# Optimization experiments

Hardware: AMD Instinct MI355X
Metric: run time of the kernel (lower is better)

## Reference

```python
import jax, jax.numpy as jnp
from jax import lax
import numpy as np

# ---- hyperparams (match init_kwargs) ----
NUM_HASHES = 8
BITS = 5
TABLE_SIZE = 64
M = 27            # ALSH augmentation length; M % (KH*KW) == 0
U = 0.83
KH = KW = 3
STRIDE = 1
PAD = 1
OUT_CHANNELS = 256
IN_CHANNELS = 64


def setup_inputs() -> dict:
    key = jax.random.key(0)
    k1, k2, k3 = jax.random.split(key, 3)
    x = jax.random.normal(k1, (32, IN_CHANNELS, 56, 56), jnp.float32)
    kernels = jax.random.normal(k2, (OUT_CHANNELS, IN_CHANNELS, KH, KW), jnp.float32) * 0.05
    a = jax.random.normal(k3, (NUM_HASHES * BITS, IN_CHANNELS * KH * KW + M), jnp.float32)
    return {"x": x, "kernels": kernels, "a": a}


def _scale_under_U(kv):
    # ScaleUnder_U: rescale all kernel vectors so max L2 norm == U
    norms = jnp.sqrt(jnp.sum(kv * kv, axis=1))
    return kv * (U / jnp.max(norms))


def _P(kv):
    # ALSH preprocessing: append ||x||^2, ||x||^4, ..., ||x||^(2^M)
    p = jnp.sum(kv * kv, axis=1, keepdims=True)  # ||x||^2
    cols = []
    for _ in range(M):
        cols.append(p)
        p = p * p
    return jnp.concatenate([kv] + cols, axis=1)  # [K, D+M]


_BIT_W = (2 ** jnp.arange(BITS)).astype(jnp.int32)


def _hash_vectors(a, v):
    # v: [K, D+M] -> bucket indices [NUM_HASHES, K]
    proj = v @ a.T                                   # [K, NUM_HASHES*BITS]
    bits = (proj > 0).astype(jnp.int32).reshape(-1, NUM_HASHES, BITS)
    idx = jnp.einsum('khb,b->hk', bits, _BIT_W)      # multi-bit SRP index
    return idx % TABLE_SIZE


def _build_table(bucket):
    # vectorized equivalent of the nested scalar-scatter loops in init_table:
    # append kernel id i to table[bucket[h, i]] in (h-major, i-minor) order.
    H, K = bucket.shape
    flat = bucket.reshape(-1)                        # [H*K]
    vals = (jnp.arange(H * K) % K).astype(jnp.int32) # stored value = kernel index i
    order = jnp.argsort(flat)                        # stable in jax
    sb, sv = flat[order], vals[order]
    pos = jnp.arange(H * K) - jnp.searchsorted(sb, sb, side='left')  # slot within bucket
    row_len = H * K
    table = jnp.zeros((TABLE_SIZE, row_len), jnp.int32).at[sb, pos].set(sv)
    lengths = jnp.zeros((TABLE_SIZE,), jnp.int32).at[flat].add(1)
    return table, lengths


def _vote_buckets(x, a):
    # Q: append M/(KH*KW) constant 1/2 planes; hash via convolution with a reshaped
    N, C, H, W = x.shape
    m_planes = M // (KH * KW)
    xq = jnp.concatenate([x, jnp.full((N, m_planes, H, W), 0.5, x.dtype)], axis=1)
    hk = a.reshape(NUM_HASHES * BITS, C + m_planes, KH, KW)  # a_to_kernel
    d = lax.conv_general_dilated(xq, hk, (STRIDE, STRIDE), [(PAD, PAD), (PAD, PAD)],
                                 dimension_numbers=('NCHW', 'OIHW', 'NCHW'))
    # [N, NUM_HASHES*BITS, H', W'] -> bucket per (hash fn, location)
    Np, _, Hp, Wp = d.shape
    bits = (d > 0).astype(jnp.int32).reshape(Np, NUM_HASHES, BITS, Hp * Wp)
    buckets = jnp.einsum('nhbs,b->hns', bits, _BIT_W) % TABLE_SIZE  # [H, N, S]
    return buckets.reshape(NUM_HASHES, -1)


def _active_mask(x, kernels, a):
    K = kernels.shape[0]
    kv = kernels.reshape(K, -1)
    buckets_k = _hash_vectors(a, _P(_scale_under_U(kv)))   # [H, K]
    table, lengths = _build_table(buckets_k)
    votes = _vote_buckets(x, a)                            # [H, N*S]
    tallied = jnp.zeros((NUM_HASHES, TABLE_SIZE), jnp.int32).at[
        jnp.arange(NUM_HASHES)[:, None], votes].add(1)     # count_votes
    indices = jnp.argmax(tallied, axis=1)                  # best bucket per hash fn
    entries = table[indices]                               # [H, row_len]
    valid = jnp.arange(table.shape[1])[None, :] < lengths[indices][:, None]
    # union of kernel ids across selected buckets (== sort+unique gather)
    mask = jnp.zeros((K,), jnp.float32).at[entries.reshape(-1)].max(
        valid.reshape(-1).astype(jnp.float32))
    return mask, tallied, indices


def reference(x, kernels, a):
    mask, tallied, indices = _active_mask(x, kernels, a)
    out = lax.conv_general_dilated(x, kernels, (STRIDE, STRIDE), [(PAD, PAD), (PAD, PAD)],
                                   dimension_numbers=('NCHW', 'OIHW', 'NCHW'))
    out = out * mask[None, :, None, None]  # conv restricted to the active kernel set
    return out, tallied, indices, mask
```

## Files before the change

### kernel.cpp

```cpp
#include <hip/hip_runtime.h>
#include <math.h>

#define NH 8
#define BITS_ 5
#define NB 40
#define TS 64
#define MAUG 27
#define CIN 64
#define HH 56
#define WW 56
#define NN 32
#define OCH 256
#define DK 576
#define DPM 603
#define HW (HH*WW)

#define CP 20
#define TILE 5440

typedef __attribute__((ext_vector_type(4))) float f32x4;
typedef __attribute__((ext_vector_type(8))) _Float16 f16x8;
typedef union { uint4 u; f16x8 h; } fragh_u;

__device__ __forceinline__ unsigned int f16b(float v) {
    union { _Float16 h; unsigned short u; } cv;
    cv.h = (_Float16)v;
    return (unsigned int)cv.u;
}
__device__ __forceinline__ float f16tof(unsigned int b) {
    union { _Float16 h; unsigned short u; } cv;
    cv.u = (unsigned short)b;
    return (float)cv.h;
}

__global__ void kP(const float* __restrict__ kern, const float* __restrict__ a,
                   float* __restrict__ aT, float* __restrict__ ctab,
                   int* __restrict__ tallied, float* __restrict__ normP,
                   unsigned short* __restrict__ whA,
                   unsigned short* __restrict__ vaH, unsigned short* __restrict__ vaL)
{
    const int bid = blockIdx.x;
    const int t = threadIdx.x;
    if (bid < 32) {
        for (int idx = bid * 256 + t; idx < DPM * NB; idx += 32 * 256) {
            int d = idx / NB, j = idx - d * NB;
            aT[idx] = a[j * DPM + d];
        }
    } else if (bid == 32) {
        for (int g = t; g < 9 * NB; g += 256) {
            int pat = g / NB, j = g - pat * NB;
            int ry = pat / 3, rx = pat % 3;
            float s = 0.f;
            for (int ky = 0; ky < 3; ++ky) {
                if (ry == 0 && ky == 0) continue;
                if (ry == 2 && ky == 2) continue;
                for (int kx = 0; kx < 3; ++kx) {
                    if (rx == 0 && kx == 0) continue;
                    if (rx == 2 && kx == 2) continue;
                    for (int mc = 0; mc < 3; ++mc)
                        s += a[j * DPM + DK + mc * 9 + ky * 3 + kx];
                }
            }
            ctab[g] = 0.5f * s;
        }
        for (int g = t; g < NH * TS; g += 256) tallied[g] = 0;
    } else if (bid < 37) {
        int g = (bid - 33) * 256 + t;
        int oc = g >> 2, part = g & 3;
        const float4* p = (const float4*)(kern + oc * DK + part * 144);
        float sq = 0.f;
        #pragma unroll 4
        for (int i = 0; i < 36; ++i) {
            float4 v = p[i];
            sq += v.x * v.x + v.y * v.y + v.z * v.z + v.w * v.w;
        }
        normP[g] = sq;
    } else {
        int idx = (bid - 37) * 256 + t;
        int f = idx >> 6, lane = idx & 63;
        if (f < 288) {
            const int kidxG = f >> 4, mf = f & 15;
            const int tap = kidxG % 9, cc = kidxG / 9;
            const int oc = mf * 16 + (lane & 15);
            const int cbase = cc * 32 + (lane >> 4) * 8;
            unsigned int hs[8];
            #pragma unroll
            for (int j = 0; j < 8; ++j)
                hs[j] = f16b(kern[oc * DK + (cbase + j) * 9 + tap]);
            unsigned int* p = (unsigned int*)(whA + ((size_t)f * 64 + lane) * 8);
            #pragma unroll
            for (int w2 = 0; w2 < 4; ++w2)
                p[w2] = hs[2 * w2] | (hs[2 * w2 + 1] << 16);
        } else if (f < 342) {
            const int fv = f - 288;
            const int kidxG = fv / 3, mfv = fv % 3;
            const int tap = kidxG % 9, cc = kidxG / 9;
            const int j = mfv * 16 + (lane & 15);
            const int cbase = cc * 32 + (lane >> 4) * 8;
            unsigned int hs[8], ls[8];
            #pragma unroll
            for (int jj = 0; jj < 8; ++jj) {
                float w = (j < NB) ? a[j * DPM + (cbase + jj) * 9 + tap] : 0.f;
                unsigned int h = f16b(w);
                unsigned int l = f16b(w - f16tof(h));
                hs[jj] = h; ls[jj] = l;
            }
            unsigned int* ph = (unsigned int*)(vaH + ((size_t)fv * 64 + lane) * 8);
            unsigned int* pl = (unsigned int*)(vaL + ((size_t)fv * 64 + lane) * 8);
            #pragma unroll
            for (int w2 = 0; w2 < 4; ++w2) {
                ph[w2] = hs[2 * w2] | (hs[2 * w2 + 1] << 16);
                pl[w2] = ls[2 * w2] | (ls[2 * w2 + 1] << 16);
            }
        }
    }
}

__global__ void __launch_bounds__(256) kH(const float* __restrict__ kern,
        const float* __restrict__ aT, const float* __restrict__ normP,
        int* __restrict__ bucket_k)
{
    __shared__ float xs[DK];
    __shared__ float red[256];
    __shared__ float accR[3 * 41];
    __shared__ float proj[NB];
    const int t = threadIdx.x;
    const int lane = t & 63, ty = t >> 6;
    const int oc = blockIdx.x;

    red[t] = fmaxf(fmaxf(normP[t], normP[t + 256]), fmaxf(normP[t + 512], normP[t + 768]));
    __syncthreads();
    for (int s = 128; s > 0; s >>= 1) {
        if (t < s) red[t] = fmaxf(red[t], red[t + s]);
        __syncthreads();
    }
    const float scale = 0.83f / sqrtf(red[0]);
    for (int i = t; i < DK; i += 256) xs[i] = scale * kern[(size_t)oc * DK + i];
    __syncthreads();

    const int j = (lane < NB) ? lane : (NB - 1);
    float acc = 0.f, sq = 0.f;
    const int d0 = ty * 144;
    for (int d = d0; d < d0 + 144; ++d) {
        float xv = xs[d];
        sq += xv * xv;
        acc += xv * aT[d * NB + j];
    }
    if (ty > 0) {
        if (lane < NB) accR[(ty - 1) * 41 + lane] = acc;
        if (lane == NB) accR[(ty - 1) * 41 + 40] = sq;
    }
    __syncthreads();
    if (ty == 0 && lane < NB) {
        acc += (accR[lane] + accR[41 + lane]) + accR[82 + lane];
        sq += (accR[40] + accR[81]) + accR[122];
        float pv = sq;
        for (int m = 0; m < MAUG; ++m) {
            acc += pv * aT[(DK + m) * NB + lane];
            pv = pv * pv;
        }
        proj[lane] = acc;
    }
    __syncthreads();
    if (t < NH) {
        int b = 0;
        #pragma unroll
        for (int bb = 0; bb < BITS_; ++bb)
            if (proj[t * BITS_ + bb] > 0.f) b |= (1 << bb);
        bucket_k[t * OCH + oc] = b & (TS - 1);
    }
}

template<int VOTE>
__global__ void __launch_bounds__(512) kM(const float* __restrict__ x,
        const unsigned short* __restrict__ whA,
        const unsigned short* __restrict__ vaH, const unsigned short* __restrict__ vaL,
        const float* __restrict__ ctab, int* __restrict__ tallied,
        const float* __restrict__ maskF, float* __restrict__ out)
{
    __shared__ unsigned int smem[2 * TILE];
    const int lane = threadIdx.x, wid = threadIdx.y;
    const int y0 = blockIdx.x * 2, n = blockIdx.y;
    const int mg = wid & 3, ng = wid >> 2;
    const int lcol = lane & 15, hi4 = lane >> 4;
    const int t = wid * 64 + lane;
    const int mfbase = VOTE ? 0 : 8;

    f32x4 acc[2][4];
    #pragma unroll
    for (int mfl = 0; mfl < 2; ++mfl)
        #pragma unroll
        for (int nf = 0; nf < 4; ++nf)
            acc[mfl][nf] = (f32x4){0.f, 0.f, 0.f, 0.f};
    f32x4 vacc[3];
    if (VOTE) {
        vacc[0] = (f32x4){0.f, 0.f, 0.f, 0.f};
        vacc[1] = (f32x4){0.f, 0.f, 0.f, 0.f};
        vacc[2] = (f32x4){0.f, 0.f, 0.f, 0.f};
    }

    if (t < 128) {
        int b = t & 3, tile = (t >> 2) & 1, li = (t >> 3) & 3, r = (t >> 5) & 3;
        int L = (li == 0) ? 0 : 64 + li;
        *(uint4*)&smem[tile * TILE + (r * 68 + L) * CP + b * 4] = make_uint4(0u, 0u, 0u, 0u);
    }

    const int q = lane;
    const int r = wid >> 1, half = wid & 1;
    const int y = y0 - 1 + r;
    const bool valid = (q < WW) && (y >= 0) && (y < HH);
    const int sbase = (r * 68 + q + 1) * CP + half * 8;

    for (int cc = 0; cc < 2; ++cc) {
        __syncthreads();
        {
            const float* xb = x + (((size_t)n * CIN + cc * 32 + half * 16) * HH +
                                   (valid ? y : 0)) * WW + q;
            #pragma unroll
            for (int u = 0; u < 2; ++u) {
                unsigned int dh[4], dl[4];
                #pragma unroll
                for (int dd = 0; dd < 4; ++dd) {
                    float v0 = valid ? xb[(size_t)(u * 8 + dd * 2) * HW] : 0.f;
                    float v1 = valid ? xb[(size_t)(u * 8 + dd * 2 + 1) * HW] : 0.f;
                    unsigned int h0 = f16b(v0), h1 = f16b(v1);
                    dh[dd] = h0 | (h1 << 16);
                    if (VOTE) {
                        unsigned int l0 = f16b(v0 - f16tof(h0));
                        unsigned int l1 = f16b(v1 - f16tof(h1));
                        dl[dd] = l0 | (l1 << 16);
                    }
                }
                *(uint4*)&smem[sbase + u * 4] = make_uint4(dh[0], dh[1], dh[2], dh[3]);
                if (VOTE)
                    *(uint4*)&smem[TILE + sbase + u * 4] = make_uint4(dl[0], dl[1], dl[2], dl[3]);
            }
        }
        __syncthreads();

        #pragma unroll
        for (int tap = 0; tap < 9; ++tap) {
            const int ky = tap / 3, kx = tap - ky * 3;
            const int kidx = cc * 9 + tap;
            fragh_u ah0, ah1;
            ah0.u = *(const uint4*)(whA + (((size_t)kidx * 16 + mfbase + mg * 2) * 64 + lane) * 8);
            ah1.u = *(const uint4*)(whA + (((size_t)kidx * 16 + mfbase + mg * 2 + 1) * 64 + lane) * 8);
            #pragma unroll
            for (int nf = 0; nf < 4; ++nf) {
                const int R = (ng + ky) * 68 + nf * 16 + lcol + kx;
                const int ad = R * CP + hi4 * 4;
                fragh_u bh;
                bh.u = *(const uint4*)&smem[ad];
                acc[0][nf] = __builtin_amdgcn_mfma_f32_16x16x32_f16(ah0.h, bh.h, acc[0][nf], 0, 0, 0);
                acc[1][nf] = __builtin_amdgcn_mfma_f32_16x16x32_f16(ah1.h, bh.h, acc[1][nf], 0, 0, 0);
                if (VOTE && nf == mg) {
                    fragh_u bl;
                    bl.u = *(const uint4*)&smem[TILE + ad];
                    #pragma unroll
                    for (int mfv = 0; mfv < 3; ++mfv) {
                        fragh_u vh, vl;
                        size_t fi = ((size_t)(kidx * 3 + mfv) * 64 + lane) * 8;
                        vh.u = *(const uint4*)(vaH + fi);
                        vl.u = *(const uint4*)(vaL + fi);
                        vacc[mfv] = __builtin_amdgcn_mfma_f32_16x16x32_f16(vh.h, bh.h, vacc[mfv], 0, 0, 0);
                        vacc[mfv] = __builtin_amdgcn_mfma_f32_16x16x32_f16(vh.h, bl.h, vacc[mfv], 0, 0, 0);
                        vacc[mfv] = __builtin_amdgcn_mfma_f32_16x16x32_f16(vl.h, bh.h, vacc[mfv], 0, 0, 0);
                    }
                }
            }
        }
    }

    const int yrow = y0 + ng;
    #pragma unroll
    for (int mfl = 0; mfl < 2; ++mfl) {
        #pragma unroll
        for (int reg = 0; reg < 4; ++reg) {
            const int oc = (mfbase + mg * 2 + mfl) * 16 + hi4 * 4 + reg;
            const float mv = VOTE ? 1.0f : maskF[oc];
            float* ob = out + (((size_t)n * OCH + oc) * HH + yrow) * WW;
            #pragma unroll
            for (int nf = 0; nf < 4; ++nf) {
                int col = nf * 16 + lcol;
                if (col < WW) ob[col] = acc[mfl][nf][reg] * mv;
            }
        }
    }

    if (VOTE) {
        __syncthreads();
        float* projT = (float*)smem;
        int* hist = (int*)&smem[8192];
        const int px = mg * 16 + lcol;
        #pragma unroll
        for (int mfv = 0; mfv < 3; ++mfv)
            #pragma unroll
            for (int reg = 0; reg < 4; ++reg)
                projT[(ng * 64 + px) * 49 + mfv * 16 + hi4 * 4 + reg] = vacc[mfv][reg];
        hist[t] = 0;
        __syncthreads();
        if (t < 2 * WW) {
            const int row = t / WW, pxx = t - row * WW;
            const int yv = y0 + row;
            const int ry = (yv == 0) ? 0 : ((yv == HH - 1) ? 2 : 1);
            const int rx = (pxx == 0) ? 0 : ((pxx == WW - 1) ? 2 : 1);
            const float* ct = ctab + (ry * 3 + rx) * NB;
            const float* pr = projT + (row * 64 + pxx) * 49;
            #pragma unroll
            for (int h = 0; h < NH; ++h) {
                int b = 0;
                #pragma unroll
                for (int bb = 0; bb < BITS_; ++bb)
                    if (pr[h * BITS_ + bb] + ct[h * BITS_ + bb] > 0.f) b |= (1 << bb);
                atomicAdd(&hist[h * TS + (b & (TS - 1))], 1);
            }
        }
        __syncthreads();
        {
            int v = hist[t];
            if (v) atomicAdd(&tallied[t], v);
        }
    }
}

__global__ void kC(const int* __restrict__ tallied, const int* __restrict__ bucket_k,
                   float* __restrict__ o_tallied, float* __restrict__ o_indices,
                   float* __restrict__ o_mask, int* __restrict__ mask_i,
                   float* __restrict__ maskF)
{
    const int t = threadIdx.x;
    __shared__ int s_idx[NH];
    if (t < NH) {
        int best = tallied[t * TS];
        int bi = 0;
        for (int b = 1; b < TS; ++b) {
            int v = tallied[t * TS + b];
            if (v > best) { best = v; bi = b; }
        }
        s_idx[t] = bi;
        o_indices[t] = (float)bi;
    }
    for (int i = t; i < NH * TS; i += 256) o_tallied[i] = (float)tallied[i];
    __syncthreads();
    int mk = 0;
    #pragma unroll
    for (int hp = 0; hp < NH; ++hp) {
        int b = bucket_k[hp * OCH + t];
        #pragma unroll
        for (int h = 0; h < NH; ++h) mk |= (b == s_idx[h]) ? 1 : 0;
    }
    mask_i[t] = mk;
    maskF[t] = (float)mk;
    o_mask[t] = (float)mk;
}

__global__ void __launch_bounds__(256) kZ(float* __restrict__ out,
                                          const int* __restrict__ mask_i)
{
    const int b = blockIdx.x;
    const int oc = b & 127;
    if (mask_i[oc]) return;
    const int n = b >> 7;
    float4* o = (float4*)(out + ((size_t)n * OCH + oc) * HW);
    for (int i = threadIdx.x; i < HW / 4; i += 256)
        o[i] = make_float4(0.f, 0.f, 0.f, 0.f);
}

extern "C" void kernel_launch(void* const* d_in, const int* in_sizes, int n_in,
                              void* d_out, int out_size, void* d_ws, size_t ws_size,
                              hipStream_t stream)
{
    const float* x    = (const float*)d_in[0];
    const float* kern = (const float*)d_in[1];
    const float* a    = (const float*)d_in[2];

    float* out       = (float*)d_out;
    float* o_tallied = out + (size_t)NN * OCH * HW;
    float* o_indices = o_tallied + NH * TS;
    float* o_mask    = o_indices + NH;

    float* ws = (float*)d_ws;
    float* aT       = ws;
    float* ctab     = ws + 24320;
    float* normP    = ws + 24704;
    int*   tallied  = (int*)(ws + 25728);
    int*   bucket_k = (int*)(ws + 26240);
    int*   mask_i   = (int*)(ws + 28288);
    float* maskF    = ws + 28544;
    unsigned short* whA = (unsigned short*)(ws + 28800);
    unsigned short* vaH = (unsigned short*)(ws + 102528);
    unsigned short* vaL = (unsigned short*)(ws + 116352);

    kP<<<123, 256, 0, stream>>>(kern, a, aT, ctab, tallied, normP, whA, vaH, vaL);
    kH<<<OCH, 256, 0, stream>>>(kern, aT, normP, bucket_k);
    kM<1><<<dim3(28, NN), dim3(64, 8), 0, stream>>>(x, whA, vaH, vaL, ctab, tallied, maskF, out);
    kC<<<1, 256, 0, stream>>>(tallied, bucket_k, o_tallied, o_indices, o_mask, mask_i, maskF);
    kM<0><<<dim3(28, NN), dim3(64, 8), 0, stream>>>(x, whA, vaH, vaL, ctab, tallied, maskF, out);
    kZ<<<NN * 128, 256, 0, stream>>>(out, mask_i);
}
```

Measured before the change: 125.3 us.

## Fuse vote and conv passes into one kernel computing all channels per row

Replaces the two-pass scheme, where a voting pass computed half the output channels and a second pass computed the rest scaled by the mask, with a single kernel. Each block now handles one output row and all 256 channels and also computes the hash-vote projections. It stages all 64 input channels in shared memory at once, with a wider padded layout. Masked-out channels are zeroed afterwards by the zeroing kernel across all 256 channels. This removes a second read of the input and the serialized second conv launch. The cost is more zero-fill writes and a reloaded halo, since each block now covers one row instead of two.

Measured after the change: 158.7 us. 26.7% more time.

```diff
diff --git a/kernel.cpp b/kernel.cpp
--- a/kernel.cpp
+++ b/kernel.cpp
@@ -15,8 +15,8 @@
 #define DPM 603
 #define HW (HH*WW)
 
-#define CP 20
-#define TILE 5440
+#define CP64 36
+#define TILE1 7344
 
 typedef __attribute__((ext_vector_type(4))) float f32x4;
 typedef __attribute__((ext_vector_type(8))) _Float16 f16x8;
@@ -171,20 +171,17 @@
     }
 }
 
-template<int VOTE>
 __global__ void __launch_bounds__(512) kM(const float* __restrict__ x,
         const unsigned short* __restrict__ whA,
         const unsigned short* __restrict__ vaH, const unsigned short* __restrict__ vaL,
         const float* __restrict__ ctab, int* __restrict__ tallied,
-        const float* __restrict__ maskF, float* __restrict__ out)
-{
-    __shared__ unsigned int smem[2 * TILE];
+        float* __restrict__ out)
+{
+    __shared__ unsigned int smem[2 * TILE1];
     const int lane = threadIdx.x, wid = threadIdx.y;
-    const int y0 = blockIdx.x * 2, n = blockIdx.y;
-    const int mg = wid & 3, ng = wid >> 2;
+    const int y0 = blockIdx.x, n = blockIdx.y;
     const int lcol = lane & 15, hi4 = lane >> 4;
     const int t = wid * 64 + lane;
-    const int mfbase = VOTE ? 0 : 8;
 
     f32x4 acc[2][4];
     #pragma unroll
@@ -192,141 +189,140 @@
         #pragma unroll
         for (int nf = 0; nf < 4; ++nf)
             acc[mfl][nf] = (f32x4){0.f, 0.f, 0.f, 0.f};
-    f32x4 vacc[3];
-    if (VOTE) {
-        vacc[0] = (f32x4){0.f, 0.f, 0.f, 0.f};
-        vacc[1] = (f32x4){0.f, 0.f, 0.f, 0.f};
-        vacc[2] = (f32x4){0.f, 0.f, 0.f, 0.f};
-    }
-
-    if (t < 128) {
-        int b = t & 3, tile = (t >> 2) & 1, li = (t >> 3) & 3, r = (t >> 5) & 3;
-        int L = (li == 0) ? 0 : 64 + li;
-        *(uint4*)&smem[tile * TILE + (r * 68 + L) * CP + b * 4] = make_uint4(0u, 0u, 0u, 0u);
-    }
-
-    const int q = lane;
-    const int r = wid >> 1, half = wid & 1;
-    const int y = y0 - 1 + r;
-    const bool valid = (q < WW) && (y >= 0) && (y < HH);
-    const int sbase = (r * 68 + q + 1) * CP + half * 8;
+    f32x4 vacc[2];
+    vacc[0] = (f32x4){0.f, 0.f, 0.f, 0.f};
+    vacc[1] = (f32x4){0.f, 0.f, 0.f, 0.f};
+    const int vnf = wid & 3;
+    const int nmf = (wid < 4) ? 2 : 1;
+
+    if (wid >= 6) {
+        int t2 = (wid - 6) * 64 + lane;
+        if (t2 < 96) {
+            int b = t2 & 7, rem = t2 >> 3;
+            int r = rem % 3, rem2 = rem / 3;
+            int L = (rem2 & 1) ? 65 : 0, tile = rem2 >> 1;
+            *(uint4*)&smem[tile * TILE1 + (r * 68 + L) * CP64 + b * 4] =
+                make_uint4(0u, 0u, 0u, 0u);
+        }
+    } else {
+        const int q = lane;
+        const int r = wid >> 1, half = wid & 1;
+        const int y = y0 - 1 + r;
+        const bool valid = (q < WW) && (y >= 0) && (y < HH);
+        const float* xb = x + (((size_t)n * CIN + half * 32) * HH + (valid ? y : 0)) * WW + q;
+        const int base = (r * 68 + q + 1) * CP64 + half * 16;
+        #pragma unroll
+        for (int u = 0; u < 4; ++u) {
+            unsigned int dh[4], dl[4];
+            #pragma unroll
+            for (int dd = 0; dd < 4; ++dd) {
+                float v0 = valid ? xb[(size_t)(u * 8 + dd * 2) * HW] : 0.f;
+                float v1 = valid ? xb[(size_t)(u * 8 + dd * 2 + 1) * HW] : 0.f;
+                unsigned int h0 = f16b(v0), h1 = f16b(v1);
+                unsigned int l0 = f16b(v0 - f16tof(h0));
+                unsigned int l1 = f16b(v1 - f16tof(h1));
+                dh[dd] = h0 | (h1 << 16);
+                dl[dd] = l0 | (l1 << 16);
+            }
+            *(uint4*)&smem[base + u * 4] = make_uint4(dh[0], dh[1], dh[2], dh[3]);
+            *(uint4*)&smem[TILE1 + base + u * 4] = make_uint4(dl[0], dl[1], dl[2], dl[3]);
+        }
+    }
+    __syncthreads();
 
     for (int cc = 0; cc < 2; ++cc) {
-        __syncthreads();
-        {
-            const float* xb = x + (((size_t)n * CIN + cc * 32 + half * 16) * HH +
-                                   (valid ? y : 0)) * WW + q;
-            #pragma unroll
-            for (int u = 0; u < 2; ++u) {
-                unsigned int dh[4], dl[4];
-                #pragma unroll
-                for (int dd = 0; dd < 4; ++dd) {
-                    float v0 = valid ? xb[(size_t)(u * 8 + dd * 2) * HW] : 0.f;
-                    float v1 = valid ? xb[(size_t)(u * 8 + dd * 2 + 1) * HW] : 0.f;
-                    unsigned int h0 = f16b(v0), h1 = f16b(v1);
-                    dh[dd] = h0 | (h1 << 16);
-                    if (VOTE) {
-                        unsigned int l0 = f16b(v0 - f16tof(h0));
-                        unsigned int l1 = f16b(v1 - f16tof(h1));
-                        dl[dd] = l0 | (l1 << 16);
-                    }
-                }
-                *(uint4*)&smem[sbase + u * 4] = make_uint4(dh[0], dh[1], dh[2], dh[3]);
-                if (VOTE)
-                    *(uint4*)&smem[TILE + sbase + u * 4] = make_uint4(dl[0], dl[1], dl[2], dl[3]);
-            }
-        }
-        __syncthreads();
-
         #pragma unroll
         for (int tap = 0; tap < 9; ++tap) {
             const int ky = tap / 3, kx = tap - ky * 3;
             const int kidx = cc * 9 + tap;
             fragh_u ah0, ah1;
-            ah0.u = *(const uint4*)(whA + (((size_t)kidx * 16 + mfbase + mg * 2) * 64 + lane) * 8);
-            ah1.u = *(const uint4*)(whA + (((size_t)kidx * 16 + mfbase + mg * 2 + 1) * 64 + lane) * 8);
+            ah0.u = *(const uint4*)(whA + (((size_t)kidx * 16 + wid * 2) * 64 + lane) * 8);
+            ah1.u = *(const uint4*)(whA + (((size_t)kidx * 16 + wid * 2 + 1) * 64 + lane) * 8);
             #pragma unroll
             for (int nf = 0; nf < 4; ++nf) {
-                const int R = (ng + ky) * 68 + nf * 16 + lcol + kx;
-                const int ad = R * CP + hi4 * 4;
+                const int ad = (ky * 68 + nf * 16 + lcol + kx) * CP64 + cc * 16 + hi4 * 4;
                 fragh_u bh;
                 bh.u = *(const uint4*)&smem[ad];
                 acc[0][nf] = __builtin_amdgcn_mfma_f32_16x16x32_f16(ah0.h, bh.h, acc[0][nf], 0, 0, 0);
                 acc[1][nf] = __builtin_amdgcn_mfma_f32_16x16x32_f16(ah1.h, bh.h, acc[1][nf], 0, 0, 0);
-                if (VOTE && nf == mg) {
+                if (nf == vnf) {
                     fragh_u bl;
-                    bl.u = *(const uint4*)&smem[TILE + ad];
+                    bl.u = *(const uint4*)&smem[TILE1 + ad];
                     #pragma unroll
-                    for (int mfv = 0; mfv < 3; ++mfv) {
-                        fragh_u vh, vl;
-                        size_t fi = ((size_t)(kidx * 3 + mfv) * 64 + lane) * 8;
-                        vh.u = *(const uint4*)(vaH + fi);
-                        vl.u = *(const uint4*)(vaL + fi);
-                        vacc[mfv] = __builtin_amdgcn_mfma_f32_16x16x32_f16(vh.h, bh.h, vacc[mfv], 0, 0, 0);
-                        vacc[mfv] = __builtin_amdgcn_mfma_f32_16x16x32_f16(vh.h, bl.h, vacc[mfv], 0, 0, 0);
-                        vacc[mfv] = __builtin_amdgcn_mfma_f32_16x16x32_f16(vl.h, bh.h, vacc[mfv], 0, 0, 0);
+                    for (int ci = 0; ci < 2; ++ci) {
+                        if (ci < nmf) {
+                            const int mfv = (wid < 4) ? ci : 2;
+                            fragh_u vh, vl;
+                            size_t fi = ((size_t)(kidx * 3 + mfv) * 64 + lane) * 8;
+                            vh.u = *(const uint4*)(vaH + fi);
+                            vl.u = *(const uint4*)(vaL + fi);
+                            vacc[ci] = __builtin_amdgcn_mfma_f32_16x16x32_f16(vh.h, bh.h, vacc[ci], 0, 0, 0);
+                            vacc[ci] = __builtin_amdgcn_mfma_f32_16x16x32_f16(vh.h, bl.h, vacc[ci], 0, 0, 0);
+                            vacc[ci] = __builtin_amdgcn_mfma_f32_16x16x32_f16(vl.h, bh.h, vacc[ci], 0, 0, 0);
+                        }
                     }
                 }
             }
         }
     }
 
-    const int yrow = y0 + ng;
     #pragma unroll
     for (int mfl = 0; mfl < 2; ++mfl) {
         #pragma unroll
         for (int reg = 0; reg < 4; ++reg) {
-            const int oc = (mfbase + mg * 2 + mfl) * 16 + hi4 * 4 + reg;
-            const float mv = VOTE ? 1.0f : maskF[oc];
-            float* ob = out + (((size_t)n * OCH + oc) * HH + yrow) * WW;
+            const int oc = (wid * 2 + mfl) * 16 + hi4 * 4 + reg;
+            float* ob = out + (((size_t)n * OCH + oc) * HH + y0) * WW;
             #pragma unroll
             for (int nf = 0; nf < 4; ++nf) {
                 int col = nf * 16 + lcol;
-                if (col < WW) ob[col] = acc[mfl][nf][reg] * mv;
-            }
-        }
-    }
-
-    if (VOTE) {
-        __syncthreads();
-        float* projT = (float*)smem;
-        int* hist = (int*)&smem[8192];
-        const int px = mg * 16 + lcol;
-        #pragma unroll
-        for (int mfv = 0; mfv < 3; ++mfv)
+                if (col < WW) ob[col] = acc[mfl][nf][reg];
+            }
+        }
+    }
+
+    __syncthreads();
+    float* projT = (float*)smem;
+    int* hist = (int*)&smem[4096];
+    {
+        const int px = vnf * 16 + lcol;
+        if (wid < 4) {
+            #pragma unroll
+            for (int ci = 0; ci < 2; ++ci)
+                #pragma unroll
+                for (int reg = 0; reg < 4; ++reg)
+                    projT[px * 49 + ci * 16 + hi4 * 4 + reg] = vacc[ci][reg];
+        } else {
             #pragma unroll
             for (int reg = 0; reg < 4; ++reg)
-                projT[(ng * 64 + px) * 49 + mfv * 16 + hi4 * 4 + reg] = vacc[mfv][reg];
-        hist[t] = 0;
-        __syncthreads();
-        if (t < 2 * WW) {
-            const int row = t / WW, pxx = t - row * WW;
-            const int yv = y0 + row;
-            const int ry = (yv == 0) ? 0 : ((yv == HH - 1) ? 2 : 1);
-            const int rx = (pxx == 0) ? 0 : ((pxx == WW - 1) ? 2 : 1);
-            const float* ct = ctab + (ry * 3 + rx) * NB;
-            const float* pr = projT + (row * 64 + pxx) * 49;
-            #pragma unroll
-            for (int h = 0; h < NH; ++h) {
-                int b = 0;
-                #pragma unroll
-                for (int bb = 0; bb < BITS_; ++bb)
-                    if (pr[h * BITS_ + bb] + ct[h * BITS_ + bb] > 0.f) b |= (1 << bb);
-                atomicAdd(&hist[h * TS + (b & (TS - 1))], 1);
-            }
-        }
-        __syncthreads();
-        {
-            int v = hist[t];
-            if (v) atomicAdd(&tallied[t], v);
-        }
+                projT[px * 49 + 32 + hi4 * 4 + reg] = vacc[0][reg];
+        }
+    }
+    hist[t] = 0;
+    __syncthreads();
+    if (t < WW) {
+        const int ry = (y0 == 0) ? 0 : ((y0 == HH - 1) ? 2 : 1);
+        const int rx = (t == 0) ? 0 : ((t == WW - 1) ? 2 : 1);
+        const float* ct = ctab + (ry * 3 + rx) * NB;
+        const float* pr = projT + t * 49;
+        #pragma unroll
+        for (int h = 0; h < NH; ++h) {
+            int b = 0;
+            #pragma unroll
+            for (int bb = 0; bb < BITS_; ++bb)
+                if (pr[h * BITS_ + bb] + ct[h * BITS_ + bb] > 0.f) b |= (1 << bb);
+            atomicAdd(&hist[h * TS + (b & (TS - 1))], 1);
+        }
+    }
+    __syncthreads();
+    {
+        int v = hist[t];
+        if (v) atomicAdd(&tallied[t], v);
     }
 }
 
 __global__ void kC(const int* __restrict__ tallied, const int* __restrict__ bucket_k,
                    float* __restrict__ o_tallied, float* __restrict__ o_indices,
-                   float* __restrict__ o_mask, int* __restrict__ mask_i,
-                   float* __restrict__ maskF)
+                   float* __restrict__ o_mask, int* __restrict__ mask_i)
 {
     const int t = threadIdx.x;
     __shared__ int s_idx[NH];
@@ -350,7 +346,6 @@
         for (int h = 0; h < NH; ++h) mk |= (b == s_idx[h]) ? 1 : 0;
     }
     mask_i[t] = mk;
-    maskF[t] = (float)mk;
     o_mask[t] = (float)mk;
 }
 
@@ -358,9 +353,9 @@
                                           const int* __restrict__ mask_i)
 {
     const int b = blockIdx.x;
-    const int oc = b & 127;
+    const int oc = b & (OCH - 1);
     if (mask_i[oc]) return;
-    const int n = b >> 7;
+    const int n = b >> 8;
     float4* o = (float4*)(out + ((size_t)n * OCH + oc) * HW);
     for (int i = threadIdx.x; i < HW / 4; i += 256)
         o[i] = make_float4(0.f, 0.f, 0.f, 0.f);
@@ -386,15 +381,13 @@
     int*   tallied  = (int*)(ws + 25728);
     int*   bucket_k = (int*)(ws + 26240);
     int*   mask_i   = (int*)(ws + 28288);
-    float* maskF    = ws + 28544;
-    unsigned short* whA = (unsigned short*)(ws + 28800);
-    unsigned short* vaH = (unsigned short*)(ws + 102528);
-    unsigned short* vaL = (unsigned short*)(ws + 116352);
+    unsigned short* whA = (unsigned short*)(ws + 28544);
+    unsigned short* vaH = (unsigned short*)(ws + 102272);
+    unsigned short* vaL = (unsigned short*)(ws + 116096);
 
     kP<<<123, 256, 0, stream>>>(kern, a, aT, ctab, tallied, normP, whA, vaH, vaL);
     kH<<<OCH, 256, 0, stream>>>(kern, aT, normP, bucket_k);
-    kM<1><<<dim3(28, NN), dim3(64, 8), 0, stream>>>(x, whA, vaH, vaL, ctab, tallied, maskF, out);
-    kC<<<1, 256, 0, stream>>>(tallied, bucket_k, o_tallied, o_indices, o_mask, mask_i, maskF);
-    kM<0><<<dim3(28, NN), dim3(64, 8), 0, stream>>>(x, whA, vaH, vaL, ctab, tallied, maskF, out);
-    kZ<<<NN * 128, 256, 0, stream>>>(out, mask_i);
-}
+    kM<<<dim3(HH, NN), dim3(64, 8), 0, stream>>>(x, whA, vaH, vaL, ctab, tallied, out);
+    kC<<<1, 256, 0, stream>>>(tallied, bucket_k, o_tallied, o_indices, o_mask, mask_i);
+    kZ<<<NN * OCH, 256, 0, stream>>>(out, mask_i);
+}
```
